# Optimization experiments

Measured on AMD Instinct MI355X. Metric: run time of the kernel, lower is better.

Reference implementation:

```python
import jax, jax.numpy as jnp
import numpy as np

QUANT_RANGE = 8
HALF_RANGE = QUANT_RANGE // 2  # 4, i.e. int4-style symmetric clamp [-4, 3]


def _find_zero_scale(t):
    zero = t.min()
    scale = (t.max() - zero) / (2 * HALF_RANGE)
    return zero, scale


def _quantize(t):
    zero, scale = _find_zero_scale(t)
    q = jnp.clip((t - zero) / scale - HALF_RANGE, -HALF_RANGE, HALF_RANGE - 1).astype(jnp.int32)
    return q, zero, scale


def setup_inputs() -> dict:
    key = jax.random.key(0)
    k1, k2, k3 = jax.random.split(key, 3)
    in_features = 4096
    out_features = 4096
    batch = 4096  # must equal out_features (shift broadcast in original module)
    x = jax.random.normal(k1, (batch, in_features), dtype=jnp.float32)
    # kaiming_uniform_(a=sqrt(5)) -> bound = 1/sqrt(in_features)
    bound = 1.0 / np.sqrt(in_features)
    weight = jax.random.uniform(k2, (out_features, in_features), dtype=jnp.float32,
                                minval=-bound, maxval=bound)
    bias = jax.random.uniform(k3, (out_features,), dtype=jnp.float32,
                              minval=-bound, maxval=bound)
    return {"x": x, "weight": weight, "bias": bias}


def reference(x, weight, bias):
    # Quantize activations and weights with global affine (min/max) quant.
    x_q, zero_act, scale_act = _quantize(x)          # [B, in], scalars
    w_q, _, _ = _quantize(weight)                    # [out, in]
    # Integer-valued GEMM (done in fp32, matching F.linear on .float() casts).
    result = x_q.astype(jnp.float32) @ w_q.astype(jnp.float32).T + bias  # [B, out]
    # Dequantize with weight-row-sum shift.
    scale_weight = (weight.max() - weight.min()) / (2 * HALF_RANGE)
    weights_reduced = weight.sum(axis=1)             # [out]
    shift = (zero_act + HALF_RANGE * scale_act) * weights_reduced[:, None]  # [out, 1]
    # NOTE: original torch code broadcasts [B,out] + [out,1]; requires B == out.
    return result * scale_act * scale_weight + shift
```

## Files before the change

kernel.cpp:

```cpp
#include <hip/hip_runtime.h>
#include <stdint.h>


using i32x4  = __attribute__((ext_vector_type(4))) int;
using i32x16 = __attribute__((ext_vector_type(16))) int;

#define TID ((int)threadIdx.x)

__global__ __launch_bounds__(256) void k_stats(const float4* __restrict__ x,
                                               const float4* __restrict__ w,
                                               float* __restrict__ pmin,
                                               float* __restrict__ pmax,
                                               float* __restrict__ wsum) {
  const int blk = blockIdx.x;
  const bool isw = blk < 4096;
  const float4* src = isw ? (w + (size_t)blk * 1024)
                          : (x + (size_t)(blk - 4096) * 1024);
  float4 v0 = src[TID], v1 = src[256 + TID], v2 = src[512 + TID], v3 = src[768 + TID];
  float lmin = fminf(fminf(fminf(v0.x, v0.y), fminf(v0.z, v0.w)),
                     fminf(fminf(v1.x, v1.y), fminf(v1.z, v1.w)));
  lmin = fminf(lmin, fminf(fminf(fminf(v2.x, v2.y), fminf(v2.z, v2.w)),
                           fminf(fminf(v3.x, v3.y), fminf(v3.z, v3.w))));
  float lmax = fmaxf(fmaxf(fmaxf(v0.x, v0.y), fmaxf(v0.z, v0.w)),
                     fmaxf(fmaxf(v1.x, v1.y), fmaxf(v1.z, v1.w)));
  lmax = fmaxf(lmax, fmaxf(fmaxf(fmaxf(v2.x, v2.y), fmaxf(v2.z, v2.w)),
                           fmaxf(fmaxf(v3.x, v3.y), fmaxf(v3.z, v3.w))));
  float lsum = ((v0.x + v0.y) + (v0.z + v0.w)) + ((v1.x + v1.y) + (v1.z + v1.w)) +
               ((v2.x + v2.y) + (v2.z + v2.w)) + ((v3.x + v3.y) + (v3.z + v3.w));

#pragma unroll
  for (int d = 32; d > 0; d >>= 1) {
    lmin = fminf(lmin, __shfl_down(lmin, d));
    lmax = fmaxf(lmax, __shfl_down(lmax, d));
    lsum += __shfl_down(lsum, d);
  }
  __shared__ float smn[4], smx[4], ssm[4];
  const int wv = TID >> 6;
  if ((TID & 63) == 0) { smn[wv] = lmin; smx[wv] = lmax; ssm[wv] = lsum; }
  __syncthreads();
  if (TID == 0) {
    float mn = fminf(fminf(smn[0], smn[1]), fminf(smn[2], smn[3]));
    float mx = fmaxf(fmaxf(smx[0], smx[1]), fmaxf(smx[2], smx[3]));
    pmin[blk] = mn; pmax[blk] = mx;
    if (isw) wsum[blk] = (ssm[0] + ssm[1]) + (ssm[2] + ssm[3]);
  }
}

__global__ __launch_bounds__(256) void k_final(const float* __restrict__ pmin,
                                               const float* __restrict__ pmax,
                                               float* __restrict__ mmf) {
  float wmn = 1e30f, wmx = -1e30f, xmn = 1e30f, xmx = -1e30f;
  for (int i = TID; i < 4096; i += 256) {
    wmn = fminf(wmn, pmin[i]);        wmx = fmaxf(wmx, pmax[i]);
    xmn = fminf(xmn, pmin[4096 + i]); xmx = fmaxf(xmx, pmax[4096 + i]);
  }
#pragma unroll
  for (int d = 32; d > 0; d >>= 1) {
    xmn = fminf(xmn, __shfl_down(xmn, d));
    xmx = fmaxf(xmx, __shfl_down(xmx, d));
    wmn = fminf(wmn, __shfl_down(wmn, d));
    wmx = fmaxf(wmx, __shfl_down(wmx, d));
  }
  __shared__ float s[4][4];
  const int wv = TID >> 6;
  if ((TID & 63) == 0) { s[wv][0] = xmn; s[wv][1] = xmx; s[wv][2] = wmn; s[wv][3] = wmx; }
  __syncthreads();
  if (TID == 0) {
    mmf[0] = fminf(fminf(s[0][0], s[1][0]), fminf(s[2][0], s[3][0]));
    mmf[1] = fmaxf(fmaxf(s[0][1], s[1][1]), fmaxf(s[2][1], s[3][1]));
    mmf[2] = fminf(fminf(s[0][2], s[1][2]), fminf(s[2][2], s[3][2]));
    mmf[3] = fmaxf(fmaxf(s[0][3], s[1][3]), fmaxf(s[2][3], s[3][3]));
  }
}

__device__ __forceinline__ int q1i(float t, float zero, float scale) {
  float v = (t - zero) / scale - 4.0f;
  v = fminf(3.0f, fmaxf(-4.0f, v));
  return (int)v;
}

__device__ __forceinline__ unsigned pack4(float4 v, float zero, float scale) {
  return (q1i(v.x, zero, scale) & 255) | ((q1i(v.y, zero, scale) & 255) << 8) |
         ((q1i(v.z, zero, scale) & 255) << 16) | ((q1i(v.w, zero, scale) & 255) << 24);
}

__global__ __launch_bounds__(256) void k_quant(const float4* __restrict__ x,
                                               const float4* __restrict__ w,
                                               uint4* __restrict__ Xq,
                                               uint4* __restrict__ Wq,
                                               const float* __restrict__ mmf) {
  bool isx = (blockIdx.x < 4096);
  int row = isx ? blockIdx.x : (blockIdx.x - 4096);
  const float4* in = (isx ? x : w) + (size_t)row * 1024 + TID * 4;
  uint4* outq = (isx ? Xq : Wq) + (size_t)row * 256 + TID;
  float zero = isx ? mmf[0] : mmf[2];
  float scale = ((isx ? mmf[1] : mmf[3]) - zero) * 0.125f;
  float4 a = in[0], b = in[1], c = in[2], d = in[3];
  uint4 o;
  o.x = pack4(a, zero, scale);
  o.y = pack4(b, zero, scale);
  o.z = pack4(c, zero, scale);
  o.w = pack4(d, zero, scale);
  *outq = o;
}

__device__ __forceinline__ void gload_lds16(const char* g, char* l) {
  __builtin_amdgcn_global_load_lds(
      (__attribute__((address_space(1))) void*)(g),
      (__attribute__((address_space(3))) void*)(l), 16, 0, 0);
}

__global__ __launch_bounds__(512, 2) void k_gemm(const char* __restrict__ Xq,
                                                 const char* __restrict__ Wq,
                                                 const float* __restrict__ bias,
                                                 const float* __restrict__ wsum,
                                                 const float* __restrict__ mmf,
                                                 float* __restrict__ out) {
  __shared__ __align__(16) char LDS[131072];

  const int tid = TID;
  const int lane = tid & 63, wave = tid >> 6;
  const int c5 = lane & 31, h = lane >> 5;
  const int wm = (wave >> 2) * 128, wn = (wave & 3) * 64;

  const int bid = (int)blockIdx.x;
  const int swz = (bid & 7) * 32 + (bid >> 3);
  const int bx = swz & 15, by = swz >> 4;
  const int brow = by * 256, bcol = bx * 256;

  const int srow = tid >> 2;
  const int lcg = (tid & 3) ^ ((tid >> 3) & 3);
  const char* gA = Xq + (size_t)(brow + srow) * 4096 + lcg * 16;
  const char* gB = Wq + (size_t)(bcol + srow) * 4096 + lcg * 16;

  const int rsw = (c5 >> 1) & 3;

  i32x16 acc[4][2];
#pragma unroll
  for (int i = 0; i < 4; ++i)
#pragma unroll
    for (int j = 0; j < 2; ++j)
#pragma unroll
      for (int e = 0; e < 16; ++e) acc[i][j][e] = 0;

#pragma unroll
  for (int kk = 0; kk < 2; ++kk) {
    char* ldA = LDS + kk * 16384 + tid * 16;
    char* ldB = LDS + 65536 + kk * 16384 + tid * 16;
    gload_lds16(gA + (size_t)kk * 64, ldA);
    gload_lds16(gA + (size_t)kk * 64 + (size_t)(128 * 4096), ldA + 8192);
    gload_lds16(gB + (size_t)kk * 64, ldB);
    gload_lds16(gB + (size_t)kk * 64 + (size_t)(128 * 4096), ldB + 8192);
  }
  __syncthreads();

#pragma unroll 2
  for (int it = 0; it < 31; ++it) {
    const int cur = it & 1, nxt = cur ^ 1;
    const int curA = cur * 32768, curB = 65536 + cur * 32768;
    const int nxtA = nxt * 32768, nxtB = 65536 + nxt * 32768;
    const size_t kOff = (size_t)(it + 1) * 128;

#pragma unroll
    for (int kk = 0; kk < 2; ++kk) {
      char* ldA = LDS + nxtA + kk * 16384 + tid * 16;
      char* ldB = LDS + nxtB + kk * 16384 + tid * 16;
      gload_lds16(gA + kOff + (size_t)kk * 64, ldA);
      gload_lds16(gA + kOff + (size_t)kk * 64 + (size_t)(128 * 4096), ldA + 8192);
      gload_lds16(gB + kOff + (size_t)kk * 64, ldB);
      gload_lds16(gB + kOff + (size_t)kk * 64 + (size_t)(128 * 4096), ldB + 8192);
    }

#pragma unroll
    for (int kk = 0; kk < 2; ++kk) {
#pragma unroll
      for (int kt = 0; kt < 2; ++kt) {
        const int pco = ((kt * 2 + h) ^ rsw) * 16;
        const int ab = curA + kk * 16384 + pco;
        const int bb = curB + kk * 16384 + pco;
        i32x4 af0 = *(const i32x4*)(LDS + ab + (wm + c5) * 64);
        i32x4 af1 = *(const i32x4*)(LDS + ab + (wm + 32 + c5) * 64);
        i32x4 af2 = *(const i32x4*)(LDS + ab + (wm + 64 + c5) * 64);
        i32x4 af3 = *(const i32x4*)(LDS + ab + (wm + 96 + c5) * 64);
        i32x4 bf0 = *(const i32x4*)(LDS + bb + (wn + c5) * 64);
        i32x4 bf1 = *(const i32x4*)(LDS + bb + (wn + 32 + c5) * 64);
        acc[0][0] = __builtin_amdgcn_mfma_i32_32x32x32_i8(af0, bf0, acc[0][0], 0, 0, 0);
        acc[0][1] = __builtin_amdgcn_mfma_i32_32x32x32_i8(af0, bf1, acc[0][1], 0, 0, 0);
        acc[1][0] = __builtin_amdgcn_mfma_i32_32x32x32_i8(af1, bf0, acc[1][0], 0, 0, 0);
        acc[1][1] = __builtin_amdgcn_mfma_i32_32x32x32_i8(af1, bf1, acc[1][1], 0, 0, 0);
        acc[2][0] = __builtin_amdgcn_mfma_i32_32x32x32_i8(af2, bf0, acc[2][0], 0, 0, 0);
        acc[2][1] = __builtin_amdgcn_mfma_i32_32x32x32_i8(af2, bf1, acc[2][1], 0, 0, 0);
        acc[3][0] = __builtin_amdgcn_mfma_i32_32x32x32_i8(af3, bf0, acc[3][0], 0, 0, 0);
        acc[3][1] = __builtin_amdgcn_mfma_i32_32x32x32_i8(af3, bf1, acc[3][1], 0, 0, 0);
      }
    }

    __syncthreads();
  }

#pragma unroll
  for (int kk = 0; kk < 2; ++kk) {
#pragma unroll
    for (int kt = 0; kt < 2; ++kt) {
      const int pco = ((kt * 2 + h) ^ rsw) * 16;
      const int ab = 32768 + kk * 16384 + pco;
      const int bb = 98304 + kk * 16384 + pco;
      i32x4 af0 = *(const i32x4*)(LDS + ab + (wm + c5) * 64);
      i32x4 af1 = *(const i32x4*)(LDS + ab + (wm + 32 + c5) * 64);
      i32x4 af2 = *(const i32x4*)(LDS + ab + (wm + 64 + c5) * 64);
      i32x4 af3 = *(const i32x4*)(LDS + ab + (wm + 96 + c5) * 64);
      i32x4 bf0 = *(const i32x4*)(LDS + bb + (wn + c5) * 64);
      i32x4 bf1 = *(const i32x4*)(LDS + bb + (wn + 32 + c5) * 64);
      acc[0][0] = __builtin_amdgcn_mfma_i32_32x32x32_i8(af0, bf0, acc[0][0], 0, 0, 0);
      acc[0][1] = __builtin_amdgcn_mfma_i32_32x32x32_i8(af0, bf1, acc[0][1], 0, 0, 0);
      acc[1][0] = __builtin_amdgcn_mfma_i32_32x32x32_i8(af1, bf0, acc[1][0], 0, 0, 0);
      acc[1][1] = __builtin_amdgcn_mfma_i32_32x32x32_i8(af1, bf1, acc[1][1], 0, 0, 0);
      acc[2][0] = __builtin_amdgcn_mfma_i32_32x32x32_i8(af2, bf0, acc[2][0], 0, 0, 0);
      acc[2][1] = __builtin_amdgcn_mfma_i32_32x32x32_i8(af2, bf1, acc[2][1], 0, 0, 0);
      acc[3][0] = __builtin_amdgcn_mfma_i32_32x32x32_i8(af3, bf0, acc[3][0], 0, 0, 0);
      acc[3][1] = __builtin_amdgcn_mfma_i32_32x32x32_i8(af3, bf1, acc[3][1], 0, 0, 0);
    }
  }

  float sa = (mmf[1] - mmf[0]) * 0.125f;
  float sw = (mmf[3] - mmf[2]) * 0.125f;
  float mid = mmf[0] + 4.0f * sa;

  const int col0 = bcol + wn + c5;
  const float b0 = bias[col0], b1 = bias[col0 + 32];
#pragma unroll
  for (int i = 0; i < 4; ++i) {
    const int rbase = brow + wm + i * 32 + 4 * h;
#pragma unroll
    for (int g = 0; g < 4; ++g) {
#pragma unroll
      for (int q = 0; q < 4; ++q) {
        const int row = rbase + 8 * g + q;
        const float shift = mid * wsum[row];
        float* po = out + (size_t)row * 4096 + col0;
        po[0]  = ((float)acc[i][0][g * 4 + q] + b0) * sa * sw + shift;
        po[32] = ((float)acc[i][1][g * 4 + q] + b1) * sa * sw + shift;
      }
    }
  }
}

extern "C" void kernel_launch(void* const* d_in, const int* in_sizes, int n_in,
                              void* d_out, int out_size, void* d_ws, size_t ws_size,
                              hipStream_t stream) {
  (void)in_sizes; (void)n_in; (void)out_size; (void)ws_size;
  const float* x = (const float*)d_in[0];
  const float* w = (const float*)d_in[1];
  const float* bias = (const float*)d_in[2];
  float* out = (float*)d_out;

  char* ws = (char*)d_ws;
  float* mmf = (float*)ws;
  float* wsum = (float*)(ws + 1024);
  float* pmin = (float*)(ws + 32768);
  float* pmax = (float*)(ws + 65536);
  char* Xq = ws + 131072;
  char* Wq = ws + 131072 + (size_t)16777216;

  k_stats<<<8192, 256, 0, stream>>>((const float4*)x, (const float4*)w, pmin, pmax, wsum);
  k_final<<<1, 256, 0, stream>>>(pmin, pmax, mmf);
  k_quant<<<8192, 256, 0, stream>>>((const float4*)x, (const float4*)w,
                                    (uint4*)Xq, (uint4*)Wq, mmf);
  k_gemm<<<256, 512, 0, stream>>>(Xq, Wq, bias, wsum, mmf, out);
}
```

Baseline: 250.3 us.

## Use 4 waves per GEMM block with 128x128 warp tiles

Cuts the GEMM block from 8 waves to 4 and gives each wave a 128x128 output tile (4x4 MFMA accumulators) instead of 128x64. B fragments loaded from LDS are reused across more MFMAs, and each thread now issues twice as many async global-to-LDS loads. This doubles accumulator registers per thread and halves the waves available to hide latency, with only one block per CU given the 128KB LDS footprint.

```diff
diff --git a/kernel.cpp b/kernel.cpp
--- a/kernel.cpp
+++ b/kernel.cpp
@@ -110,7 +110,7 @@
       (__attribute__((address_space(3))) void*)(l), 16, 0, 0);
 }
 
-__global__ __launch_bounds__(512, 2) void k_gemm(const char* __restrict__ Xq,
+__global__ __launch_bounds__(256, 1) void k_gemm(const char* __restrict__ Xq,
                                                  const char* __restrict__ Wq,
                                                  const float* __restrict__ bias,
                                                  const float* __restrict__ wsum,
@@ -121,7 +121,7 @@
   const int tid = TID;
   const int lane = tid & 63, wave = tid >> 6;
   const int c5 = lane & 31, h = lane >> 5;
-  const int wm = (wave >> 2) * 128, wn = (wave & 3) * 64;
+  const int wm = (wave >> 1) * 128, wn = (wave & 1) * 128;
 
   const int bid = (int)blockIdx.x;
   const int swz = (bid & 7) * 32 + (bid >> 3);
@@ -135,22 +135,23 @@
 
   const int rsw = (c5 >> 1) & 3;
 
-  i32x16 acc[4][2];
+  i32x16 acc[4][4];
 #pragma unroll
   for (int i = 0; i < 4; ++i)
 #pragma unroll
-    for (int j = 0; j < 2; ++j)
+    for (int j = 0; j < 4; ++j)
 #pragma unroll
       for (int e = 0; e < 16; ++e) acc[i][j][e] = 0;
 
 #pragma unroll
   for (int kk = 0; kk < 2; ++kk) {
-    char* ldA = LDS + kk * 16384 + tid * 16;
-    char* ldB = LDS + 65536 + kk * 16384 + tid * 16;
-    gload_lds16(gA + (size_t)kk * 64, ldA);
-    gload_lds16(gA + (size_t)kk * 64 + (size_t)(128 * 4096), ldA + 8192);
-    gload_lds16(gB + (size_t)kk * 64, ldB);
-    gload_lds16(gB + (size_t)kk * 64 + (size_t)(128 * 4096), ldB + 8192);
+#pragma unroll
+    for (int g = 0; g < 4; ++g) {
+      gload_lds16(gA + (size_t)kk * 64 + (size_t)g * (64 * 4096),
+                  LDS + kk * 16384 + g * 4096 + tid * 16);
+      gload_lds16(gB + (size_t)kk * 64 + (size_t)g * (64 * 4096),
+                  LDS + 65536 + kk * 16384 + g * 4096 + tid * 16);
+    }
   }
   __syncthreads();
 
@@ -163,12 +164,13 @@
 
 #pragma unroll
     for (int kk = 0; kk < 2; ++kk) {
-      char* ldA = LDS + nxtA + kk * 16384 + tid * 16;
-      char* ldB = LDS + nxtB + kk * 16384 + tid * 16;
-      gload_lds16(gA + kOff + (size_t)kk * 64, ldA);
-      gload_lds16(gA + kOff + (size_t)kk * 64 + (size_t)(128 * 4096), ldA + 8192);
-      gload_lds16(gB + kOff + (size_t)kk * 64, ldB);
-      gload_lds16(gB + kOff + (size_t)kk * 64 + (size_t)(128 * 4096), ldB + 8192);
+#pragma unroll
+      for (int g = 0; g < 4; ++g) {
+        gload_lds16(gA + kOff + (size_t)kk * 64 + (size_t)g * (64 * 4096),
+                    LDS + nxtA + kk * 16384 + g * 4096 + tid * 16);
+        gload_lds16(gB + kOff + (size_t)kk * 64 + (size_t)g * (64 * 4096),
+                    LDS + nxtB + kk * 16384 + g * 4096 + tid * 16);
+      }
     }
 
 #pragma unroll
@@ -184,14 +186,16 @@
         i32x4 af3 = *(const i32x4*)(LDS + ab + (wm + 96 + c5) * 64);
         i32x4 bf0 = *(const i32x4*)(LDS + bb + (wn + c5) * 64);
         i32x4 bf1 = *(const i32x4*)(LDS + bb + (wn + 32 + c5) * 64);
-        acc[0][0] = __builtin_amdgcn_mfma_i32_32x32x32_i8(af0, bf0, acc[0][0], 0, 0, 0);
-        acc[0][1] = __builtin_amdgcn_mfma_i32_32x32x32_i8(af0, bf1, acc[0][1], 0, 0, 0);
-        acc[1][0] = __builtin_amdgcn_mfma_i32_32x32x32_i8(af1, bf0, acc[1][0], 0, 0, 0);
-        acc[1][1] = __builtin_amdgcn_mfma_i32_32x32x32_i8(af1, bf1, acc[1][1], 0, 0, 0);
-        acc[2][0] = __builtin_amdgcn_mfma_i32_32x32x32_i8(af2, bf0, acc[2][0], 0, 0, 0);
-        acc[2][1] = __builtin_amdgcn_mfma_i32_32x32x32_i8(af2, bf1, acc[2][1], 0, 0, 0);
-        acc[3][0] = __builtin_amdgcn_mfma_i32_32x32x32_i8(af3, bf0, acc[3][0], 0, 0, 0);
-        acc[3][1] = __builtin_amdgcn_mfma_i32_32x32x32_i8(af3, bf1, acc[3][1], 0, 0, 0);
+        i32x4 bf2 = *(const i32x4*)(LDS + bb + (wn + 64 + c5) * 64);
+        i32x4 bf3 = *(const i32x4*)(LDS + bb + (wn + 96 + c5) * 64);
+#pragma unroll
+        for (int i = 0; i < 4; ++i) {
+          const i32x4 af = (i == 0) ? af0 : (i == 1) ? af1 : (i == 2) ? af2 : af3;
+          acc[i][0] = __builtin_amdgcn_mfma_i32_32x32x32_i8(af, bf0, acc[i][0], 0, 0, 0);
+          acc[i][1] = __builtin_amdgcn_mfma_i32_32x32x32_i8(af, bf1, acc[i][1], 0, 0, 0);
+          acc[i][2] = __builtin_amdgcn_mfma_i32_32x32x32_i8(af, bf2, acc[i][2], 0, 0, 0);
+          acc[i][3] = __builtin_amdgcn_mfma_i32_32x32x32_i8(af, bf3, acc[i][3], 0, 0, 0);
+        }
       }
     }
 
@@ -211,14 +215,16 @@
       i32x4 af3 = *(const i32x4*)(LDS + ab + (wm + 96 + c5) * 64);
       i32x4 bf0 = *(const i32x4*)(LDS + bb + (wn + c5) * 64);
       i32x4 bf1 = *(const i32x4*)(LDS + bb + (wn + 32 + c5) * 64);
-      acc[0][0] = __builtin_amdgcn_mfma_i32_32x32x32_i8(af0, bf0, acc[0][0], 0, 0, 0);
-      acc[0][1] = __builtin_amdgcn_mfma_i32_32x32x32_i8(af0, bf1, acc[0][1], 0, 0, 0);
-      acc[1][0] = __builtin_amdgcn_mfma_i32_32x32x32_i8(af1, bf0, acc[1][0], 0, 0, 0);
-      acc[1][1] = __builtin_amdgcn_mfma_i32_32x32x32_i8(af1, bf1, acc[1][1], 0, 0, 0);
-      acc[2][0] = __builtin_amdgcn_mfma_i32_32x32x32_i8(af2, bf0, acc[2][0], 0, 0, 0);
-      acc[2][1] = __builtin_amdgcn_mfma_i32_32x32x32_i8(af2, bf1, acc[2][1], 0, 0, 0);
-      acc[3][0] = __builtin_amdgcn_mfma_i32_32x32x32_i8(af3, bf0, acc[3][0], 0, 0, 0);
-      acc[3][1] = __builtin_amdgcn_mfma_i32_32x32x32_i8(af3, bf1, acc[3][1], 0, 0, 0);
+      i32x4 bf2 = *(const i32x4*)(LDS + bb + (wn + 64 + c5) * 64);
+      i32x4 bf3 = *(const i32x4*)(LDS + bb + (wn + 96 + c5) * 64);
+#pragma unroll
+      for (int i = 0; i < 4; ++i) {
+        const i32x4 af = (i == 0) ? af0 : (i == 1) ? af1 : (i == 2) ? af2 : af3;
+        acc[i][0] = __builtin_amdgcn_mfma_i32_32x32x32_i8(af, bf0, acc[i][0], 0, 0, 0);
+        acc[i][1] = __builtin_amdgcn_mfma_i32_32x32x32_i8(af, bf1, acc[i][1], 0, 0, 0);
+        acc[i][2] = __builtin_amdgcn_mfma_i32_32x32x32_i8(af, bf2, acc[i][2], 0, 0, 0);
+        acc[i][3] = __builtin_amdgcn_mfma_i32_32x32x32_i8(af, bf3, acc[i][3], 0, 0, 0);
+      }
     }
   }
 
@@ -227,7 +233,8 @@
   float mid = mmf[0] + 4.0f * sa;
 
   const int col0 = bcol + wn + c5;
-  const float b0 = bias[col0], b1 = bias[col0 + 32];
+  const float b0 = bias[col0],      b1 = bias[col0 + 32];
+  const float b2 = bias[col0 + 64], b3 = bias[col0 + 96];
 #pragma unroll
   for (int i = 0; i < 4; ++i) {
     const int rbase = brow + wm + i * 32 + 4 * h;
@@ -240,6 +247,8 @@
         float* po = out + (size_t)row * 4096 + col0;
         po[0]  = ((float)acc[i][0][g * 4 + q] + b0) * sa * sw + shift;
         po[32] = ((float)acc[i][1][g * 4 + q] + b1) * sa * sw + shift;
+        po[64] = ((float)acc[i][2][g * 4 + q] + b2) * sa * sw + shift;
+        po[96] = ((float)acc[i][3][g * 4 + q] + b3) * sa * sw + shift;
       }
     }
   }
@@ -266,5 +275,5 @@
   k_final<<<1, 256, 0, stream>>>(pmin, pmax, mmf);
   k_quant<<<8192, 256, 0, stream>>>((const float4*)x, (const float4*)w,
                                     (uint4*)Xq, (uint4*)Wq, mmf);
-  k_gemm<<<256, 512, 0, stream>>>(Xq, Wq, bias, wsum, mmf, out);
-}
+  k_gemm<<<256, 256, 0, stream>>>(Xq, Wq, bias, wsum, mmf, out);
+}
```

Result: slower. 257.6 us (+2.9%).
